# Kernel tuning notes

Hardware: AMD Instinct MI355X
Metric: run time of the kernel (lower is better)

## Reference

```python
import jax, jax.numpy as jnp
import numpy as np

B, S, D, H, G = 2, 4096, 768, 12, 64
HD = D // H
W = 256              # one-sided window (attention_window=512); also the chunk size
NC = S // W
NEG = -1e9
SCALE = 1.0 / np.sqrt(HD)


def setup_inputs() -> dict:
    key = jax.random.key(0)
    ks = jax.random.split(key, 9)
    lin = lambda k: 0.02 * jax.random.normal(k, (D, D), dtype=jnp.float32)
    zb = lambda: jnp.zeros((D,), jnp.float32)
    return {
        "query": jax.random.normal(ks[0], (S, B, D), dtype=jnp.float32),
        # 0 = local token, -1 = global token (wrapper multiplies by -1 -> +1 = global in HF convention)
        "key_padding_mask": jnp.zeros((B, S), jnp.int32).at[:, :G].set(-1),
        "Wq": lin(ks[1]), "bq": zb(),
        "Wk": lin(ks[2]), "bk": zb(),
        "Wv": lin(ks[3]), "bv": zb(),
        "Wqg": lin(ks[4]), "bqg": zb(),
        "Wkg": lin(ks[5]), "bkg": zb(),
        "Wvg": lin(ks[6]), "bvg": zb(),
        "Wo": lin(ks[7]), "bo": zb(),
    }


def _heads(x):  # [B,S,D] -> [B,H,S,HD]
    return x.reshape(B, S, H, HD).transpose(0, 2, 1, 3)


def reference(query, key_padding_mask, Wq, bq, Wk, bk, Wv, bv,
              Wqg, bqg, Wkg, bkg, Wvg, bvg, Wo, bo):
    x = query.transpose(1, 0, 2)                      # [B,S,D]
    attn_mask = -key_padding_mask                     # wrapper: key_padding_mask * -1
    is_pad = attn_mask < 0                            # [B,S]
    is_glb = attn_mask > 0

    q = _heads(x @ Wq + bq) * SCALE                   # [B,H,S,HD]
    k = _heads(x @ Wk + bk)
    v = _heads(x @ Wv + bv)

    # ---- sliding-window scores via overlapping 3-chunk key blocks ----
    qc = q.reshape(B, H, NC, W, HD)
    blk_idx = jnp.arange(NC)[:, None] * W + jnp.arange(3 * W)[None, :]   # [NC,3W] into padded seq
    kpad = jnp.pad(k, ((0, 0), (0, 0), (W, W), (0, 0)))
    vpad = jnp.pad(v, ((0, 0), (0, 0), (W, W), (0, 0)))
    kblk = kpad[:, :, blk_idx]                        # [B,H,NC,3W,HD]
    vblk = vpad[:, :, blk_idx]
    local = jnp.einsum('bhcqd,bhckd->bhcqk', qc, kblk)  # [B,H,NC,W,3W]

    rel = jnp.arange(3 * W)[None, :] - jnp.arange(W)[:, None] - W        # key pos - query pos
    jpos = (jnp.arange(NC)[:, None, None] - 1) * W + jnp.arange(3 * W)[None, None, :]
    band_ok = (jnp.abs(rel)[None] <= W) & (jpos >= 0) & (jpos < S)       # [NC,W,3W]

    key_bad = is_pad | is_glb                         # pad keys masked; global keys handled separately
    kb_blk = jnp.pad(key_bad, ((0, 0), (W, W)), constant_values=True)[:, blk_idx]  # [B,NC,3W]
    ok = band_ok[None, None] & ~kb_blk[:, None, :, None, :]
    local = jnp.where(ok, local, NEG)

    # ---- all queries -> global keys (first G tokens), regular K/V ----
    gsc = jnp.einsum('bhqd,bhgd->bhqg', q, k[:, :, :G])                  # [B,H,S,G]

    scores = jnp.concatenate([gsc, local.reshape(B, H, S, 3 * W)], axis=-1)
    probs = jax.nn.softmax(scores, axis=-1)
    pg = probs[..., :G]
    pl = probs[..., G:].reshape(B, H, NC, W, 3 * W)

    out = jnp.einsum('bhcqk,bhckd->bhcqd', pl, vblk).reshape(B, H, S, HD)
    out = out + jnp.einsum('bhqg,bhgd->bhqd', pg, v[:, :, :G])

    # ---- global query rows: full attention with the dedicated global projections ----
    qg = (_heads(x @ Wqg + bqg) * SCALE)[:, :, :G]    # [B,H,G,HD]
    kg = _heads(x @ Wkg + bkg)
    vg = _heads(x @ Wvg + bvg)
    gq = jnp.einsum('bhgd,bhkd->bhgk', qg, kg)        # [B,H,G,S]
    gq = jnp.where(is_pad[:, None, None, :], NEG, gq)
    gp = jax.nn.softmax(gq, axis=-1)
    out = out.at[:, :, :G].set(jnp.einsum('bhgk,bhkd->bhgd', gp, vg))

    attn_out = out.transpose(0, 2, 1, 3).reshape(B, S, D)   # merge heads -> [B,S,D]
    attn_out = attn_out.transpose(1, 0, 2)                  # back to [S,B,D]
    return attn_out @ Wo + bo                               # wrapper's output Linear
```

## Files before the change

kernel.cpp:

```cpp
#include <hip/hip_runtime.h>
#include <hip/hip_bf16.h>
#include <cstdint>

#define BB 2
#define SS 4096
#define DD 768
#define HH 12
#define GG 64
#define WW 256

typedef __hip_bfloat16 bf16;
typedef unsigned short u16;
typedef __attribute__((ext_vector_type(8))) short short8v;
typedef __attribute__((ext_vector_type(4))) float floatx4;
typedef __attribute__((ext_vector_type(16))) float floatx16;

__device__ __forceinline__ float b2f(u16 u) {
  return __uint_as_float(((unsigned int)u) << 16);
}
__device__ __forceinline__ u16 f2bu(float f) {
  bf16 h = __float2bfloat16(f);
  return *reinterpret_cast<u16*>(&h);
}
__device__ __forceinline__ void async_copy16(const u16* g, u16* l) {
  __builtin_amdgcn_global_load_lds(
      (const __attribute__((address_space(1))) void*)g,
      (__attribute__((address_space(3))) void*)l, 16, 0, 0);
}

struct P7 { const void* p[7]; };

__global__ __launch_bounds__(256) void detect_dtype(const u16* __restrict__ q,
                                                    int* __restrict__ flag) {
  __shared__ int cnt;
  int tid = threadIdx.x;
  if (tid == 0) cnt = 0;
  __syncthreads();
  int bad = 0;
#pragma unroll
  for (int i = 0; i < 16; ++i) {
    float f = b2f(q[tid * 16 + i]);
    if (!isfinite(f) || fabsf(f) > 100.f) bad++;
  }
  atomicAdd(&cnt, bad);
  __syncthreads();
  if (tid == 0) *flag = (cnt > 256) ? 1 : 0;
}

__global__ __launch_bounds__(256) void prep(P7 wsrc, P7 bsrc,
                                            const void* __restrict__ qsrc,
                                            bf16* __restrict__ cWt,
                                            bf16* __restrict__ cB,
                                            bf16* __restrict__ cQ,
                                            const int* __restrict__ flag) {
  bool f32 = (*flag != 0);
  int z = blockIdx.z;
  if (z < 7) {
    __shared__ float tile[32][33];
    const void* src = wsrc.p[z];
    bf16* d = cWt + (size_t)z * DD * DD;
    int tx = threadIdx.x & 31, ty = threadIdx.x >> 5;
    int k0 = blockIdx.x * 32, n0 = blockIdx.y * 32;
#pragma unroll
    for (int i = 0; i < 32; i += 8) {
      int k = k0 + ty + i, n = n0 + tx;
      float v = f32 ? ((const float*)src)[(size_t)k * DD + n]
                    : b2f(((const u16*)src)[(size_t)k * DD + n]);
      tile[ty + i][tx] = v;
    }
    __syncthreads();
#pragma unroll
    for (int i = 0; i < 32; i += 8) {
      int n = n0 + ty + i, k = k0 + tx;
      d[(size_t)n * DD + k] = __float2bfloat16(tile[tx][ty + i]);
    }
  } else if (z == 7) {
    int bidx = blockIdx.x + 24 * blockIdx.y;
    const int n = BB * HH * SS * 64;
    for (int i = bidx * 256 + threadIdx.x; i < n; i += 576 * 256) {
      float v = f32 ? ((const float*)qsrc)[i] : b2f(((const u16*)qsrc)[i]);
      cQ[i] = __float2bfloat16(v);
    }
  } else {
    int which = blockIdx.x;
    if (which >= 7 || blockIdx.y != 0) return;
    const void* s = bsrc.p[which];
    for (int j = threadIdx.x; j < DD; j += 256)
      cB[which * DD + j] =
          __float2bfloat16(f32 ? ((const float*)s)[j] : b2f(((const u16*)s)[j]));
  }
}

__global__ __launch_bounds__(256) void tr_vt2(const bf16* __restrict__ s0,
                                              bf16* __restrict__ d0,
                                              const bf16* __restrict__ s1,
                                              bf16* __restrict__ d1) {
  __shared__ u16 T[64][66];
  int stile = blockIdx.x, bh = blockIdx.y;
  const u16* in = (const u16*)(blockIdx.z ? s1 : s0) + (size_t)bh * SS * 64;
  u16* out = (u16*)(blockIdx.z ? d1 : d0) + (size_t)bh * SS * 64;
  int tid = threadIdx.x;
  int srow = tid >> 2, scol = (tid & 3) * 16;
#pragma unroll
  for (int i = 0; i < 4; ++i) {
    ushort4 u = *(const ushort4*)(in + (size_t)(stile * 64 + srow) * 64 + scol + 4 * i);
    *(ushort2*)&T[srow][scol + 4 * i] = make_ushort2(u.x, u.y);
    *(ushort2*)&T[srow][scol + 4 * i + 2] = make_ushort2(u.z, u.w);
  }
  __syncthreads();
#pragma unroll
  for (int i = 0; i < 4; ++i) {
    ushort4 u;
    u.x = T[scol + 4 * i + 0][srow];
    u.y = T[scol + 4 * i + 1][srow];
    u.z = T[scol + 4 * i + 2][srow];
    u.w = T[scol + 4 * i + 3][srow];
    *(ushort4*)(out + (size_t)srow * SS + stile * 64 + scol + 4 * i) = u;
  }
}

__device__ __forceinline__ void stage_tile(const u16* __restrict__ gp,
                                           size_t row0, u16 (*Ls)[64], int w,
                                           int lane, int k0) {
#pragma unroll
  for (int j = 0; j < 4; ++j)
    async_copy16(gp + (row0 + (size_t)(w * 32 + j * 8 + (lane >> 3))) * DD + k0 +
                     (((lane & 7) ^ ((lane >> 3) & 7)) << 3),
                 &Ls[w * 32 + j * 8][0]);
}
__device__ __forceinline__ short8v lda(u16 (*Ls)[64], int base, int lane, int kk) {
  int row = base + (lane & 31);
  int c = (kk >> 3) + (lane >> 5);
  return *(const short8v*)&Ls[row][((c ^ (row & 7)) << 3)];
}

__device__ __forceinline__ void gemm_core2(const u16* __restrict__ Xp,
                                           const u16* __restrict__ Wp, int bm,
                                           int bn, int tid, u16 (*As)[64],
                                           u16 (*Bs)[64], floatx16 (&acc)[2][2]) {
  int lane = tid & 63, w = tid >> 6;
  int wm = (w >> 1) * 64, wn = (w & 1) * 64;
  for (int k0 = 0; k0 < DD; k0 += 64) {
    __syncthreads();
    stage_tile(Wp, (size_t)bn, As, w, lane, k0);
    stage_tile(Xp, (size_t)bm, Bs, w, lane, k0);
    __syncthreads();
#pragma unroll
    for (int kk = 0; kk < 64; kk += 16) {
      short8v a0 = lda(As, wn, lane, kk);
      short8v a1 = lda(As, wn + 32, lane, kk);
      short8v b0 = lda(Bs, wm, lane, kk);
      short8v b1 = lda(Bs, wm + 32, lane, kk);
      acc[0][0] = __builtin_amdgcn_mfma_f32_32x32x16_bf16(a0, b0, acc[0][0], 0, 0, 0);
      acc[0][1] = __builtin_amdgcn_mfma_f32_32x32x16_bf16(a0, b1, acc[0][1], 0, 0, 0);
      acc[1][0] = __builtin_amdgcn_mfma_f32_32x32x16_bf16(a1, b0, acc[1][0], 0, 0, 0);
      acc[1][1] = __builtin_amdgcn_mfma_f32_32x32x16_bf16(a1, b1, acc[1][1], 0, 0, 0);
    }
  }
}

__global__ __launch_bounds__(256, 4) void gemm5(const bf16* __restrict__ Xb,
                                                const bf16* __restrict__ Wt0,
                                                const bf16* __restrict__ b0,
                                                bf16* __restrict__ out0,
                                                bf16* __restrict__ qg) {
  __shared__ __align__(16) u16 As[128][64];
  __shared__ __align__(16) u16 Bs[128][64];
  int tid = threadIdx.x, lane = tid & 63, w = tid >> 6;
  int wm = (w >> 1) * 64, wn = (w & 1) * 64;
  int which, bn, bm;
  if (blockIdx.y == 30) {
    if (blockIdx.x >= 6) return;
    which = 5;
    bn = blockIdx.x * 128;
    bm = 0;
  } else {
    which = blockIdx.y / 6;
    bn = (blockIdx.y % 6) * 128;
    bm = blockIdx.x * 128;
  }
  const u16* Wp = (const u16*)Wt0 + (size_t)which * DD * DD;
  const u16* bias = (const u16*)b0 + which * DD;
  int Sdim = (which == 5) ? GG : SS;
  u16* outp = (which == 5) ? (u16*)qg
                           : (u16*)out0 + (size_t)which * BB * HH * SS * 64;
  float scale = (which == 0 || which == 5) ? 0.125f : 1.f;
  floatx16 acc[2][2];
#pragma unroll
  for (int i = 0; i < 2; ++i)
#pragma unroll
    for (int j = 0; j < 2; ++j) acc[i][j] = (floatx16)(0.f);
  gemm_core2((const u16*)Xb, Wp, bm, bn, tid, As, Bs, acc);
#pragma unroll
  for (int nt = 0; nt < 2; ++nt) {
    int n0 = bn + wn + nt * 32;
    int h = n0 >> 6;
    int nsub = (n0 & 63) + ((lane >> 5) << 2);
    ushort4 bi[4];
#pragma unroll
    for (int g = 0; g < 4; ++g)
      bi[g] = *(const ushort4*)&bias[n0 + ((lane >> 5) << 2) + g * 8];
#pragma unroll
    for (int mt = 0; mt < 2; ++mt) {
      int m = bm + wm + mt * 32 + (lane & 31);
      int s = m >> 1, b = m & 1;
      u16* outb = outp + ((size_t)(b * HH + h) * Sdim + s) * 64 + nsub;
#pragma unroll
      for (int g = 0; g < 4; ++g) {
        ushort4 o;
        o.x = f2bu((acc[nt][mt][4 * g + 0] + b2f(bi[g].x)) * scale);
        o.y = f2bu((acc[nt][mt][4 * g + 1] + b2f(bi[g].y)) * scale);
        o.z = f2bu((acc[nt][mt][4 * g + 2] + b2f(bi[g].z)) * scale);
        o.w = f2bu((acc[nt][mt][4 * g + 3] + b2f(bi[g].w)) * scale);
        *(ushort4*)(outb + g * 8) = o;
      }
    }
  }
}

__global__ __launch_bounds__(256, 4) void gemm_out(const bf16* __restrict__ Xb,
                                                   const bf16* __restrict__ Wtb,
                                                   const bf16* __restrict__ biasb,
                                                   float* __restrict__ outv) {
  __shared__ __align__(16) u16 As[128][64];
  __shared__ __align__(16) u16 Bs[128][64];
  int tid = threadIdx.x, lane = tid & 63, w = tid >> 6;
  int wm = (w >> 1) * 64, wn = (w & 1) * 64;
  int bm = blockIdx.x * 128, bn = blockIdx.y * 128;
  floatx16 acc[2][2];
#pragma unroll
  for (int i = 0; i < 2; ++i)
#pragma unroll
    for (int j = 0; j < 2; ++j) acc[i][j] = (floatx16)(0.f);
  gemm_core2((const u16*)Xb, (const u16*)Wtb, bm, bn, tid, As, Bs, acc);
  const u16* bias = (const u16*)biasb;
#pragma unroll
  for (int nt = 0; nt < 2; ++nt) {
    int n0 = bn + wn + nt * 32 + ((lane >> 5) << 2);
    ushort4 bi[4];
#pragma unroll
    for (int g = 0; g < 4; ++g) bi[g] = *(const ushort4*)&bias[n0 + g * 8];
#pragma unroll
    for (int mt = 0; mt < 2; ++mt) {
      int m = bm + wm + mt * 32 + (lane & 31);
      float* outb = outv + (size_t)m * DD + n0;
#pragma unroll
      for (int g = 0; g < 4; ++g) {
        float4 o;
        o.x = acc[nt][mt][4 * g + 0] + b2f(bi[g].x);
        o.y = acc[nt][mt][4 * g + 1] + b2f(bi[g].y);
        o.z = acc[nt][mt][4 * g + 2] + b2f(bi[g].z);
        o.w = acc[nt][mt][4 * g + 3] + b2f(bi[g].w);
        *(float4*)(outb + g * 8) = o;
      }
    }
  }
}

__global__ __launch_bounds__(256, 3) void attn_local128(
    const bf16* __restrict__ qb, const bf16* __restrict__ kb,
    const bf16* __restrict__ vtb, const int* __restrict__ kpm,
    bf16* __restrict__ attnout) {
  __shared__ __align__(16) u16 Qs[128][64];
  __shared__ __align__(16) u16 Ks[64][64];
  __shared__ __align__(16) u16 Vt[64][64];
  __shared__ __align__(16) u16 Ps[128][72];
  __shared__ float Ls[128];
  __shared__ int kbadS[64];
  int bid = blockIdx.x;
  int tile = bid & 31, bh = bid >> 5;
  int b = bh / HH, h = bh % HH;
  int tid = threadIdx.x, lane = tid & 63, w = tid >> 6;
  int quad = lane >> 4, t = lane & 15;
  const u16* qp = (const u16*)qb + (size_t)bh * SS * 64;
  const u16* kp = (const u16*)kb + (size_t)bh * SS * 64;
  const u16* vp = (const u16*)vtb + (size_t)bh * SS * 64;
  int sq0 = GG + tile * 128;
#pragma unroll
  for (int j = 0; j < 4; ++j) {
    int qr = sq0 + w * 32 + j * 8 + (lane >> 3);
    int sr = qr < SS ? qr : SS - 1;
    async_copy16(qp + (size_t)sr * 64 + (lane & 7) * 8, &Qs[w * 32 + j * 8][0]);
  }
  __syncthreads();
  short8v aq[2][2];
#pragma unroll
  for (int st = 0; st < 2; ++st)
#pragma unroll
    for (int ks = 0; ks < 2; ++ks)
      aq[st][ks] = *(const short8v*)&Qs[w * 32 + st * 16 + t][ks * 32 + quad * 8];
  floatx4 O[2][4];
#pragma unroll
  for (int st = 0; st < 2; ++st)
#pragma unroll
    for (int dt = 0; dt < 4; ++dt) O[st][dt] = (floatx4)(0.f);
  float ps[2][4] = {};
  int win_lo = max(sq0 - WW, GG);
  int win_hi = min(sq0 + 127 + WW, SS - 1);
  int kb_lo = win_lo & ~63;
  int iters = ((win_hi - kb_lo) >> 6) + 2;
  for (int it = 0; it < iters; ++it) {
    int kbs = (it == 0) ? 0 : kb_lo + ((it - 1) << 6);
    __syncthreads();
#pragma unroll
    for (int j = 0; j < 2; ++j) {
      async_copy16(kp + (size_t)(kbs + w * 16 + j * 8 + (lane >> 3)) * 64 +
                       (lane & 7) * 8,
                   &Ks[w * 16 + j * 8][0]);
      async_copy16(vp + (size_t)(w * 16 + j * 8 + (lane >> 3)) * SS + kbs +
                       (lane & 7) * 8,
                   &Vt[w * 16 + j * 8][0]);
    }
    if (tid < 64) kbadS[tid] = kpm[b * SS + kbs + tid];
    __syncthreads();
#pragma unroll
    for (int st = 0; st < 2; ++st) {
      floatx4 S[4];
#pragma unroll
      for (int nt = 0; nt < 4; ++nt) {
        S[nt] = (floatx4)(0.f);
#pragma unroll
        for (int ks = 0; ks < 2; ++ks) {
          short8v bk = *(const short8v*)&Ks[nt * 16 + t][ks * 32 + quad * 8];
          S[nt] = __builtin_amdgcn_mfma_f32_16x16x32_bf16(aq[st][ks], bk, S[nt],
                                                          0, 0, 0);
        }
      }
      int prow = w * 32 + st * 16 + quad * 4;
      if (it == 0) {
#pragma unroll
        for (int nt = 0; nt < 4; ++nt)
#pragma unroll
          for (int r = 0; r < 4; ++r) {
            float p = __expf(S[nt][r]);
            ps[st][r] += p;
            Ps[prow + r][((nt ^ quad) << 4) + t] = f2bu(p);
          }
      } else {
#pragma unroll
        for (int r = 0; r < 4; ++r) {
          int qr = sq0 + prow + r;
          int off = kbs + t + WW - qr;
#pragma unroll
          for (int nt = 0; nt < 4; ++nt) {
            int bad = kbadS[nt * 16 + t];
            unsigned u = (unsigned)(off + nt * 16);
            float p = __expf((u <= 2 * WW && bad == 0) ? S[nt][r] : -3.0e38f);
            ps[st][r] += p;
            Ps[prow + r][((nt ^ quad) << 4) + t] = f2bu(p);
          }
        }
      }
    }
    short8v ap[2][2];
#pragma unroll
    for (int st = 0; st < 2; ++st)
#pragma unroll
      for (int ks = 0; ks < 2; ++ks) {
        int chunk = (2 * ks + (quad >> 1)) ^ ((t >> 2) & 3);
        ap[st][ks] = *(const short8v*)&Ps[w * 32 + st * 16 + t]
                                        [(chunk << 4) + ((quad & 1) << 3)];
      }
#pragma unroll
    for (int dt = 0; dt < 4; ++dt) {
#pragma unroll
      for (int ks = 0; ks < 2; ++ks) {
        short8v av = *(const short8v*)&Vt[dt * 16 + t][ks * 32 + quad * 8];
#pragma unroll
        for (int st = 0; st < 2; ++st)
          O[st][dt] = __builtin_amdgcn_mfma_f32_16x16x32_bf16(av, ap[st][ks],
                                                              O[st][dt], 0, 0, 0);
      }
    }
  }
#pragma unroll
  for (int st = 0; st < 2; ++st) {
#pragma unroll
    for (int r = 0; r < 4; ++r)
#pragma unroll
      for (int off = 1; off < 16; off <<= 1) ps[st][r] += __shfl_xor(ps[st][r], off);
    if (t == 0)
#pragma unroll
      for (int r = 0; r < 4; ++r) Ls[w * 32 + st * 16 + quad * 4 + r] = ps[st][r];
  }
#pragma unroll
  for (int st = 0; st < 2; ++st) {
    int q = sq0 + w * 32 + st * 16 + t;
    if (q < SS) {
      float linv = 1.0f / Ls[w * 32 + st * 16 + t];
#pragma unroll
      for (int dt = 0; dt < 4; ++dt) {
        ushort4 o;
        o.x = f2bu(O[st][dt][0] * linv);
        o.y = f2bu(O[st][dt][1] * linv);
        o.z = f2bu(O[st][dt][2] * linv);
        o.w = f2bu(O[st][dt][3] * linv);
        *(ushort4*)((u16*)attnout + ((size_t)q * BB + b) * DD + h * 64 +
                    dt * 16 + quad * 4) = o;
      }
    }
  }
}

__global__ __launch_bounds__(256) void attn_glb(
    const bf16* __restrict__ qgb, const bf16* __restrict__ kgb,
    const bf16* __restrict__ vtb, const int* __restrict__ kpm,
    float* __restrict__ part) {
  __shared__ __align__(16) u16 Qs[64][72];
  __shared__ __align__(16) u16 Ks[64][72];
  __shared__ __align__(16) u16 Vt[64][72];
  __shared__ __align__(16) u16 Ps[64][72];
  __shared__ int kbadS[64];
  int bid = blockIdx.x;
  int bh = bid >> 4, seg = bid & 15;
  int b = bh / HH;
  int tid = threadIdx.x, lane = tid & 63, w = tid >> 6;
  int quad = lane >> 4, t = lane & 15;
  const u16* qp = (const u16*)qgb + (size_t)bh * GG * 64;
  const u16* kp = (const u16*)kgb + (size_t)bh * SS * 64;
  const u16* vp = (const u16*)vtb + (size_t)bh * SS * 64;
  int srow = tid >> 2, scol = (tid & 3) * 16;
#pragma unroll
  for (int i = 0; i < 4; ++i)
    *(ushort4*)&Qs[srow][scol + 4 * i] =
        *(const ushort4*)(qp + (size_t)srow * 64 + scol + 4 * i);
  __syncthreads();
  short8v aq[2];
#pragma unroll
  for (int ks = 0; ks < 2; ++ks)
    aq[ks] = *(const short8v*)&Qs[16 * w + t][ks * 32 + quad * 8];
  floatx4 O[4];
#pragma unroll
  for (int i = 0; i < 4; ++i) O[i] = (floatx4)(0.f);
  float ps[4] = {0.f, 0.f, 0.f, 0.f};
  for (int it = 0; it < 4; ++it) {
    int kbs = (seg << 8) + (it << 6);
    ushort4 ku[4], vu[4];
#pragma unroll
    for (int i = 0; i < 4; ++i) {
      ku[i] = *(const ushort4*)(kp + (size_t)(kbs + srow) * 64 + scol + 4 * i);
      vu[i] = *(const ushort4*)(vp + (size_t)srow * SS + kbs + scol + 4 * i);
    }
    int kbval = (tid < 64) ? kpm[b * SS + kbs + tid] : 0;
    __syncthreads();
#pragma unroll
    for (int i = 0; i < 4; ++i) {
      *(ushort4*)&Ks[srow][scol + 4 * i] = ku[i];
      *(ushort4*)&Vt[srow][scol + 4 * i] = vu[i];
    }
    if (tid < 64) kbadS[tid] = kbval;
    __syncthreads();
    floatx4 S[4];
#pragma unroll
    for (int nt = 0; nt < 4; ++nt) {
      S[nt] = (floatx4)(0.f);
#pragma unroll
      for (int ks = 0; ks < 2; ++ks) {
        short8v bk = *(const short8v*)&Ks[nt * 16 + t][ks * 32 + quad * 8];
        S[nt] = __builtin_amdgcn_mfma_f32_16x16x32_bf16(aq[ks], bk, S[nt], 0, 0, 0);
      }
    }
#pragma unroll
    for (int nt = 0; nt < 4; ++nt) {
      int bad = kbadS[nt * 16 + t];
#pragma unroll
      for (int r = 0; r < 4; ++r) {
        float p = __expf((bad <= 0) ? S[nt][r] : -3.0e38f);
        ps[r] += p;
        Ps[16 * w + quad * 4 + r][((nt ^ quad) << 4) + t] = f2bu(p);
      }
    }
    short8v ap[2];
#pragma unroll
    for (int ks = 0; ks < 2; ++ks) {
      int chunk = (2 * ks + (quad >> 1)) ^ ((t >> 2) & 3);
      ap[ks] = *(const short8v*)&Ps[16 * w + t][(chunk << 4) + ((quad & 1) << 3)];
    }
#pragma unroll
    for (int dt = 0; dt < 4; ++dt)
#pragma unroll
      for (int ks = 0; ks < 2; ++ks) {
        short8v bv = *(const short8v*)&Vt[dt * 16 + t][ks * 32 + quad * 8];
        O[dt] = __builtin_amdgcn_mfma_f32_16x16x32_bf16(ap[ks], bv, O[dt], 0, 0, 0);
      }
  }
#pragma unroll
  for (int r = 0; r < 4; ++r)
#pragma unroll
    for (int off = 1; off < 16; off <<= 1) ps[r] += __shfl_xor(ps[r], off);
  float* pO = part + (size_t)bid * 4160;
#pragma unroll
  for (int dt = 0; dt < 4; ++dt)
#pragma unroll
    for (int r = 0; r < 4; ++r)
      pO[(16 * w + quad * 4 + r) * 64 + dt * 16 + t] = O[dt][r];
  if (t == 0)
#pragma unroll
    for (int r = 0; r < 4; ++r) pO[4096 + 16 * w + quad * 4 + r] = ps[r];
}

__global__ __launch_bounds__(256) void attn_comb(const float* __restrict__ part,
                                                 bf16* __restrict__ attnout) {
  int tid = threadIdx.x, lane = tid & 63, w = tid >> 6;
  int idx = blockIdx.x * 4 + w;
  int bh = idx >> 6, row = idx & 63;
  int b = bh / HH, h = bh % HH;
  float o = 0.f, L = 0.f;
#pragma unroll
  for (int s16 = 0; s16 < 16; ++s16) {
    const float* p = part + (size_t)(bh * 16 + s16) * 4160;
    o += p[(row << 6) + lane];
    L += p[4096 + row];
  }
  attnout[((size_t)row * BB + b) * DD + h * 64 + lane] = __float2bfloat16(o / L);
}

extern "C" void kernel_launch(void* const* d_in, const int* in_sizes, int n_in,
                              void* d_out, int out_size, void* d_ws,
                              size_t ws_size, hipStream_t stream) {
  const int* kpm = (const int*)d_in[1];
  float* outp = (float*)d_out;
  const size_t SZ = (size_t)BB * HH * SS * 64;
  const size_t WSZ = (size_t)DD * DD;
  bf16* p = (bf16*)d_ws;
  bf16* cQ = p; p += SZ;
  bf16* cWt = p; p += 7 * WSZ;
  bf16* cB = p; p += 7 * DD;
  bf16* q = p; p += SZ;
  bf16* k = p; p += SZ;
  bf16* v = p; p += SZ;
  bf16* kg = p; p += SZ;
  bf16* vg = p; p += SZ;
  bf16* qg = p; p += (size_t)BB * HH * GG * 64;
  bf16* attnout = p; p += SZ;
  float* part = (float*)p;
  int* flag = (int*)(part + (size_t)384 * 4160);
  bf16* vT = cQ;
  bf16* vgT = v;
  dim3 blk(256);
  (void)kg; (void)vg;

  P7 wsrc{{d_in[2], d_in[4], d_in[6], d_in[10], d_in[12], d_in[8], d_in[14]}};
  P7 bsrc{{d_in[3], d_in[5], d_in[7], d_in[11], d_in[13], d_in[9], d_in[15]}};

  detect_dtype<<<1, blk, 0, stream>>>((const u16*)d_in[0], flag);
  prep<<<dim3(24, 24, 9), blk, 0, stream>>>(wsrc, bsrc, d_in[0], cWt, cB, cQ, flag);
  gemm5<<<dim3(64, 31), blk, 0, stream>>>(cQ, cWt, cB, q, qg);
  tr_vt2<<<dim3(64, 24, 2), blk, 0, stream>>>(v, vT, vg, vgT);
  attn_local128<<<dim3(24 * 32), blk, 0, stream>>>(q, k, vT, kpm, attnout);
  attn_glb<<<dim3(BB * HH * 16), blk, 0, stream>>>(qg, kg, vgT, kpm, part);
  attn_comb<<<dim3(BB * HH * 16), blk, 0, stream>>>(part, attnout);
  gemm_out<<<dim3(64, 6), blk, 0, stream>>>(attnout, cWt + 6 * WSZ, cB + 6 * DD, outp);
}
```

Measured before the change: 300.7 us.

## Enlarge QKV projection GEMM tile to 256 rows and fold log2e into query scale

The fused projection GEMM now uses 256x128 output tiles with each wave owning 64 rows and four 32-column fragments, which halves the grid and reuses each weight tile across more rows. Launch bounds drop to 2 blocks per SM to make room for the larger accumulator set. The query scale now includes log2(e), so the attention kernels can call exp2f instead of __expf. The costs are lower occupancy, more LDS per block, and a guard that skips out-of-range rows for the small global-query projection.

```diff
diff --git a/kernel.cpp b/kernel.cpp
--- a/kernel.cpp
+++ b/kernel.cpp
@@ -14,6 +14,8 @@
 typedef __attribute__((ext_vector_type(8))) short short8v;
 typedef __attribute__((ext_vector_type(4))) float floatx4;
 typedef __attribute__((ext_vector_type(16))) float floatx16;
+
+#define QSCALE 0.18033688011112042f
 
 __device__ __forceinline__ float b2f(u16 u) {
   return __uint_as_float(((unsigned int)u) << 16);
@@ -119,19 +121,46 @@
   }
 }
 
-__device__ __forceinline__ void stage_tile(const u16* __restrict__ gp,
-                                           size_t row0, u16 (*Ls)[64], int w,
-                                           int lane, int k0) {
-#pragma unroll
-  for (int j = 0; j < 4; ++j)
-    async_copy16(gp + (row0 + (size_t)(w * 32 + j * 8 + (lane >> 3))) * DD + k0 +
-                     (((lane & 7) ^ ((lane >> 3) & 7)) << 3),
-                 &Ls[w * 32 + j * 8][0]);
-}
 __device__ __forceinline__ short8v lda(u16 (*Ls)[64], int base, int lane, int kk) {
   int row = base + (lane & 31);
   int c = (kk >> 3) + (lane >> 5);
   return *(const short8v*)&Ls[row][((c ^ (row & 7)) << 3)];
+}
+
+__device__ __forceinline__ void gemm_core3(const u16* __restrict__ Xp,
+                                           const u16* __restrict__ Wp, int bm,
+                                           int bn, int tid, u16 (*As)[64],
+                                           u16 (*Bs)[64], floatx16 (&acc)[4][2]) {
+  int lane = tid & 63, w = tid >> 6;
+  int wm = w * 64;
+  int r8 = lane >> 3;
+  int sw = (((lane & 7) ^ (r8 & 7)) << 3);
+  for (int k0 = 0; k0 < DD; k0 += 64) {
+    __syncthreads();
+#pragma unroll
+    for (int j = 0; j < 4; ++j)
+      async_copy16(Wp + (size_t)(bn + w * 32 + j * 8 + r8) * DD + k0 + sw,
+                   &As[w * 32 + j * 8][0]);
+#pragma unroll
+    for (int j = 0; j < 8; ++j)
+      async_copy16(Xp + (size_t)(bm + w * 64 + j * 8 + r8) * DD + k0 + sw,
+                   &Bs[w * 64 + j * 8][0]);
+    __syncthreads();
+#pragma unroll
+    for (int kk = 0; kk < 64; kk += 16) {
+      short8v a[4], b[2];
+#pragma unroll
+      for (int nf = 0; nf < 4; ++nf) a[nf] = lda(As, nf * 32, lane, kk);
+#pragma unroll
+      for (int mf = 0; mf < 2; ++mf) b[mf] = lda(Bs, wm + mf * 32, lane, kk);
+#pragma unroll
+      for (int nf = 0; nf < 4; ++nf)
+#pragma unroll
+        for (int mf = 0; mf < 2; ++mf)
+          acc[nf][mf] = __builtin_amdgcn_mfma_f32_32x32x16_bf16(
+              a[nf], b[mf], acc[nf][mf], 0, 0, 0);
+    }
+  }
 }
 
 __device__ __forceinline__ void gemm_core2(const u16* __restrict__ Xp,
@@ -140,10 +169,17 @@
                                            u16 (*Bs)[64], floatx16 (&acc)[2][2]) {
   int lane = tid & 63, w = tid >> 6;
   int wm = (w >> 1) * 64, wn = (w & 1) * 64;
+  int r8 = lane >> 3;
+  int sw = (((lane & 7) ^ (r8 & 7)) << 3);
   for (int k0 = 0; k0 < DD; k0 += 64) {
     __syncthreads();
-    stage_tile(Wp, (size_t)bn, As, w, lane, k0);
-    stage_tile(Xp, (size_t)bm, Bs, w, lane, k0);
+#pragma unroll
+    for (int j = 0; j < 4; ++j) {
+      async_copy16(Wp + (size_t)(bn + w * 32 + j * 8 + r8) * DD + k0 + sw,
+                   &As[w * 32 + j * 8][0]);
+      async_copy16(Xp + (size_t)(bm + w * 32 + j * 8 + r8) * DD + k0 + sw,
+                   &Bs[w * 32 + j * 8][0]);
+    }
     __syncthreads();
 #pragma unroll
     for (int kk = 0; kk < 64; kk += 16) {
@@ -159,15 +195,14 @@
   }
 }
 
-__global__ __launch_bounds__(256, 4) void gemm5(const bf16* __restrict__ Xb,
+__global__ __launch_bounds__(256, 2) void gemm5(const bf16* __restrict__ Xb,
                                                 const bf16* __restrict__ Wt0,
                                                 const bf16* __restrict__ b0,
                                                 bf16* __restrict__ out0,
                                                 bf16* __restrict__ qg) {
   __shared__ __align__(16) u16 As[128][64];
-  __shared__ __align__(16) u16 Bs[128][64];
+  __shared__ __align__(16) u16 Bs[256][64];
   int tid = threadIdx.x, lane = tid & 63, w = tid >> 6;
-  int wm = (w >> 1) * 64, wn = (w & 1) * 64;
   int which, bn, bm;
   if (blockIdx.y == 30) {
     if (blockIdx.x >= 6) return;
@@ -177,42 +212,38 @@
   } else {
     which = blockIdx.y / 6;
     bn = (blockIdx.y % 6) * 128;
-    bm = blockIdx.x * 128;
+    bm = blockIdx.x * 256;
   }
   const u16* Wp = (const u16*)Wt0 + (size_t)which * DD * DD;
   const u16* bias = (const u16*)b0 + which * DD;
   int Sdim = (which == 5) ? GG : SS;
   u16* outp = (which == 5) ? (u16*)qg
                            : (u16*)out0 + (size_t)which * BB * HH * SS * 64;
-  float scale = (which == 0 || which == 5) ? 0.125f : 1.f;
-  floatx16 acc[2][2];
-#pragma unroll
-  for (int i = 0; i < 2; ++i)
+  float scale = (which == 0 || which == 5) ? QSCALE : 1.f;
+  floatx16 acc[4][2];
+#pragma unroll
+  for (int i = 0; i < 4; ++i)
 #pragma unroll
     for (int j = 0; j < 2; ++j) acc[i][j] = (floatx16)(0.f);
-  gemm_core2((const u16*)Xb, Wp, bm, bn, tid, As, Bs, acc);
-#pragma unroll
-  for (int nt = 0; nt < 2; ++nt) {
-    int n0 = bn + wn + nt * 32;
-    int h = n0 >> 6;
-    int nsub = (n0 & 63) + ((lane >> 5) << 2);
-    ushort4 bi[4];
-#pragma unroll
-    for (int g = 0; g < 4; ++g)
-      bi[g] = *(const ushort4*)&bias[n0 + ((lane >> 5) << 2) + g * 8];
-#pragma unroll
-    for (int mt = 0; mt < 2; ++mt) {
-      int m = bm + wm + mt * 32 + (lane & 31);
-      int s = m >> 1, b = m & 1;
-      u16* outb = outp + ((size_t)(b * HH + h) * Sdim + s) * 64 + nsub;
-#pragma unroll
-      for (int g = 0; g < 4; ++g) {
+  gemm_core3((const u16*)Xb, Wp, bm, bn, tid, As, Bs, acc);
+#pragma unroll
+  for (int nf = 0; nf < 4; ++nf) {
+#pragma unroll
+    for (int g = 0; g < 4; ++g) {
+      int nbase = bn + nf * 32 + g * 8 + ((lane >> 5) << 2);
+      int h = nbase >> 6, nsub = nbase & 63;
+      ushort4 bi = *(const ushort4*)&bias[nbase];
+#pragma unroll
+      for (int mf = 0; mf < 2; ++mf) {
+        int m = bm + w * 64 + mf * 32 + (lane & 31);
+        int s = m >> 1, b = m & 1;
+        if (which == 5 && s >= GG) continue;
         ushort4 o;
-        o.x = f2bu((acc[nt][mt][4 * g + 0] + b2f(bi[g].x)) * scale);
-        o.y = f2bu((acc[nt][mt][4 * g + 1] + b2f(bi[g].y)) * scale);
-        o.z = f2bu((acc[nt][mt][4 * g + 2] + b2f(bi[g].z)) * scale);
-        o.w = f2bu((acc[nt][mt][4 * g + 3] + b2f(bi[g].w)) * scale);
-        *(ushort4*)(outb + g * 8) = o;
+        o.x = f2bu((acc[nf][mf][4 * g + 0] + b2f(bi.x)) * scale);
+        o.y = f2bu((acc[nf][mf][4 * g + 1] + b2f(bi.y)) * scale);
+        o.z = f2bu((acc[nf][mf][4 * g + 2] + b2f(bi.z)) * scale);
+        o.w = f2bu((acc[nf][mf][4 * g + 3] + b2f(bi.w)) * scale);
+        *(ushort4*)(outp + ((size_t)(b * HH + h) * Sdim + s) * 64 + nsub) = o;
       }
     }
   }
@@ -332,7 +363,7 @@
         for (int nt = 0; nt < 4; ++nt)
 #pragma unroll
           for (int r = 0; r < 4; ++r) {
-            float p = __expf(S[nt][r]);
+            float p = exp2f(S[nt][r]);
             ps[st][r] += p;
             Ps[prow + r][((nt ^ quad) << 4) + t] = f2bu(p);
           }
@@ -345,7 +376,7 @@
           for (int nt = 0; nt < 4; ++nt) {
             int bad = kbadS[nt * 16 + t];
             unsigned u = (unsigned)(off + nt * 16);
-            float p = __expf((u <= 2 * WW && bad == 0) ? S[nt][r] : -3.0e38f);
+            float p = exp2f((u <= 2 * WW && bad == 0) ? S[nt][r] : -3.0e38f);
             ps[st][r] += p;
             Ps[prow + r][((nt ^ quad) << 4) + t] = f2bu(p);
           }
@@ -465,7 +496,7 @@
       int bad = kbadS[nt * 16 + t];
 #pragma unroll
       for (int r = 0; r < 4; ++r) {
-        float p = __expf((bad <= 0) ? S[nt][r] : -3.0e38f);
+        float p = exp2f((bad <= 0) ? S[nt][r] : -3.0e38f);
         ps[r] += p;
         Ps[16 * w + quad * 4 + r][((nt ^ quad) << 4) + t] = f2bu(p);
       }
@@ -545,7 +576,7 @@
 
   detect_dtype<<<1, blk, 0, stream>>>((const u16*)d_in[0], flag);
   prep<<<dim3(24, 24, 9), blk, 0, stream>>>(wsrc, bsrc, d_in[0], cWt, cB, cQ, flag);
-  gemm5<<<dim3(64, 31), blk, 0, stream>>>(cQ, cWt, cB, q, qg);
+  gemm5<<<dim3(32, 31), blk, 0, stream>>>(cQ, cWt, cB, q, qg);
   tr_vt2<<<dim3(64, 24, 2), blk, 0, stream>>>(v, vT, vg, vgT);
   attn_local128<<<dim3(24 * 32), blk, 0, stream>>>(q, k, vT, kpm, attnout);
   attn_glb<<<dim3(BB * HH * 16), blk, 0, stream>>>(qg, kg, vgT, kpm, part);
```

New measurement: 294.2 us. 2.2% less time.
